# Kernel optimization log

Hardware: AMD Instinct MI355X
Metric: run time of the kernel (lower is better)

Reference implementation:

```python
import jax, jax.numpy as jnp
import numpy as np

B, A, D = 32, 1024, 128
THR = 0.05  # proximity_threshold


def setup_inputs() -> dict:
    key = jax.random.key(0)
    k1, k2, k3, k4, k5 = jax.random.split(key, 5)
    s = 1.0 / np.sqrt(D)
    return {
        "agent_embeds": jax.random.normal(k1, (B, A, D), jnp.float32),
        "agent_coords": jax.random.uniform(k2, (B, A, 2), jnp.float32),
        "agent_mask": jax.random.randint(k3, (B, A), 0, 2).astype(jnp.int32),
        "W1": (jax.random.normal(k4, (D, D), jnp.float32) * s),
        "b1": jnp.zeros((D,), jnp.float32),
        "W2": (jax.random.normal(k5, (D, D), jnp.float32) * s),
        "b2": jnp.zeros((D,), jnp.float32),
    }


def _cluster(coords, valid):
    """Greedy sequential proximity clustering (same order/semantics as the torch loop).
    coords [A,2], valid [A] bool -> assigned [A] int32 (group id; invalid agents = -2)."""
    diff = coords[:, None, :] - coords[None, :, :]          # [A,A,2]
    near_all = jnp.sum(diff * diff, axis=-1) < (THR * THR)   # dist < thr  <=>  dist^2 < thr^2
    assigned0 = jnp.where(valid, -1, -2).astype(jnp.int32)

    def step(carry, i):
        assigned, gid = carry
        start = assigned[i] == -1                 # valid and not yet assigned -> new group
        take = start & near_all[i] & (assigned == -1)  # includes i (dist ii = 0)
        assigned = jnp.where(take, gid, assigned)
        gid = gid + start.astype(jnp.int32)
        return (assigned, gid), None

    (assigned, _), _ = jax.lax.scan(step, (assigned0, jnp.int32(0)), jnp.arange(A))
    return assigned


def reference(agent_embeds, agent_coords, agent_mask, W1, b1, W2, b2):
    valid = agent_mask.astype(bool)                          # [B,A]
    assigned = jax.vmap(_cluster)(agent_coords, valid)       # [B,A] int32

    w = valid.astype(agent_embeds.dtype)                     # [B,A]
    seg = jnp.where(valid, assigned, 0)                      # invalid -> seg 0 with weight 0

    def pool(emb, sg, wt):  # per batch: segment-mean into at most A groups (padded)
        sums = jax.ops.segment_sum(emb * wt[:, None], sg, num_segments=A)  # [A,D]
        cnt = jax.ops.segment_sum(wt, sg, num_segments=A)                  # [A]
        return sums / jnp.maximum(cnt, 1.0)[:, None], cnt > 0

    group_tokens, group_mask = jax.vmap(pool)(agent_embeds, seg, w)  # [B,A,D], [B,A]

    # group_proj MLP applied to the whole (zero-padded) token tensor, as in torch
    h = jax.nn.gelu(group_tokens @ W1 + b1, approximate=False)
    group_tokens = h @ W2 + b2

    agent_to_group = jnp.where(valid, assigned, -1)
    return group_tokens, group_mask, agent_to_group
```

## Files before the change

### kernel.cpp

```cpp
#include <hip/hip_runtime.h>
#include <hip/hip_bf16.h>

#define NB 32
#define NA 1024
#define ND 128
#define TG 16

__device__ __forceinline__ float gelu_exact(float x) {
    return 0.5f * x * (1.0f + erff(x * 0.7071067811865476f));
}

__global__ __launch_bounds__(64, 1) void cluster_kernel(
    const float2* __restrict__ coords, const int* __restrict__ mask,
    int* __restrict__ assigned, int* __restrict__ gcount,
    float* __restrict__ out_mask, float* __restrict__ out_a2g,
    const float* __restrict__ b1, const float* __restrict__ W2,
    const float* __restrict__ b2, float* __restrict__ empty_row)
{
    const int lane = threadIdx.x;

    if (blockIdx.x == NB) {
        __shared__ float h0s[ND];
        h0s[lane]      = gelu_exact(b1[lane]);
        h0s[lane + 64] = gelu_exact(b1[lane + 64]);
        __syncthreads();
        float a0 = b2[lane], a1 = b2[lane + 64];
        for (int k = 0; k < ND; ++k) {
            float h = h0s[k];
            a0 += h * W2[k * ND + lane];
            a1 += h * W2[k * ND + lane + 64];
        }
        empty_row[lane]      = a0;
        empty_row[lane + 64] = a1;
        return;
    }

    const int b = blockIdx.x;
    const float2* cb = coords + (b << 10);
    const int*    mb = mask + (b << 10);

    float2 cxy[16];
    int asg[16];
    unsigned m = 0;
#pragma unroll
    for (int s = 0; s < 16; ++s) {
        cxy[s] = cb[s * 64 + lane];
        int v = mb[s * 64 + lane];
        asg[s] = v ? -1 : -2;
        m |= (v ? 1u : 0u) << s;
    }

    const float thr2 = 0.05f * 0.05f;
    int gid = 0;
#pragma unroll
    for (int s = 0; s < 16; ++s) {
        unsigned long long cand = __ballot((m >> s) & 1u);
        while (cand) {
            int L = (int)__builtin_ctzll(cand);
            float lx = __builtin_bit_cast(float,
                __builtin_amdgcn_readlane(__builtin_bit_cast(int, cxy[s].x), L));
            float ly = __builtin_bit_cast(float,
                __builtin_amdgcn_readlane(__builtin_bit_cast(int, cxy[s].y), L));
            unsigned take = 0u;
#pragma unroll
            for (int t = s; t < 16; ++t) {
                float dx = cxy[t].x - lx;
                float dy = cxy[t].y - ly;
                float d2 = __fadd_rn(__fmul_rn(dx, dx), __fmul_rn(dy, dy));
                bool tk = (d2 < thr2) && ((m >> t) & 1u);
                if (tk) asg[t] = gid;
                take |= (tk ? 1u : 0u) << t;
            }
            m &= ~take;
            ++gid;
            cand = __ballot((m >> s) & 1u);
        }
    }

    int*   ab = assigned + (b << 10);
    float* o2 = out_a2g + (b << 10);
    float* o1 = out_mask + (b << 10);
#pragma unroll
    for (int s = 0; s < 16; ++s) {
        int i = s * 64 + lane;
        ab[i] = asg[s];
        o2[i] = (asg[s] == -2) ? -1.0f : (float)asg[s];
        o1[i] = (i < gid) ? 1.0f : 0.0f;
    }
    if (lane == 0) gcount[b] = gid;
}

__global__ __launch_bounds__(256) void csr_kernel(
    const int* __restrict__ assigned,
    int* __restrict__ memb, int* __restrict__ goff, float* __restrict__ gcntf)
{
    const int b = blockIdx.x;
    const int tid = threadIdx.x;
    __shared__ int cnt[NA];
    __shared__ int sA[NA];
    __shared__ int sB[NA];
    __shared__ int cur[NA];

    for (int i = tid; i < NA; i += 256) cnt[i] = 0;
    __syncthreads();

    const int4 av = ((const int4*)(assigned + (b << 10)))[tid];
    if (av.x >= 0) atomicAdd(&cnt[av.x], 1);
    if (av.y >= 0) atomicAdd(&cnt[av.y], 1);
    if (av.z >= 0) atomicAdd(&cnt[av.z], 1);
    if (av.w >= 0) atomicAdd(&cnt[av.w], 1);
    __syncthreads();

    for (int i = tid; i < NA; i += 256) sA[i] = cnt[i];
    __syncthreads();
    int* src = sA; int* dst = sB;
    for (int d = 1; d < NA; d <<= 1) {
        for (int i = tid; i < NA; i += 256) {
            int v = src[i];
            if (i >= d) v += src[i - d];
            dst[i] = v;
        }
        __syncthreads();
        int* t = src; src = dst; dst = t;
    }
    for (int i = tid; i < NA; i += 256) cur[i] = src[i] - cnt[i];
    __syncthreads();
    for (int i = tid; i < NA; i += 256) {
        goff[(b << 10) + i]  = cur[i];
        gcntf[(b << 10) + i] = (float)cnt[i];
    }
    __syncthreads();

    const int a = tid * 4;
    if (av.x >= 0) { int p = atomicAdd(&cur[av.x], 1); memb[(b << 10) + p] = a; }
    if (av.y >= 0) { int p = atomicAdd(&cur[av.y], 1); memb[(b << 10) + p] = a + 1; }
    if (av.z >= 0) { int p = atomicAdd(&cur[av.z], 1); memb[(b << 10) + p] = a + 2; }
    if (av.w >= 0) { int p = atomicAdd(&cur[av.w], 1); memb[(b << 10) + p] = a + 3; }
}

__global__ __launch_bounds__(256) void token_kernel(
    const float* __restrict__ emb, const int* __restrict__ memb,
    const int* __restrict__ goff, const float* __restrict__ gcntf,
    const int* __restrict__ gcount, float* __restrict__ tokens)
{
    const int b = blockIdx.y;
    if (blockIdx.x * TG >= gcount[b]) return;
    const int g = blockIdx.x * TG + (threadIdx.x >> 4);
    const int sub = threadIdx.x & 15;

    const int off = goff[(b << 10) + g];
    const int n   = (int)gcntf[(b << 10) + g];
    const int* mb = memb + (b << 10) + off;
    const float* eb = emb + ((size_t)(b << 10)) * ND + sub * 8;

    float acc[8];
#pragma unroll
    for (int j = 0; j < 8; ++j) acc[j] = 0.0f;
    for (int k = 0; k < n; ++k) {
        int a = mb[k];
        const float4* e4 = (const float4*)(eb + (size_t)a * ND);
        float4 v0 = e4[0], v1 = e4[1];
        acc[0] += v0.x; acc[1] += v0.y; acc[2] += v0.z; acc[3] += v0.w;
        acc[4] += v1.x; acc[5] += v1.y; acc[6] += v1.z; acc[7] += v1.w;
    }
    const float den = fmaxf((float)n, 1.0f);
    float4 t0, t1;
    t0.x = acc[0] / den; t0.y = acc[1] / den; t0.z = acc[2] / den; t0.w = acc[3] / den;
    t1.x = acc[4] / den; t1.y = acc[5] / den; t1.z = acc[6] / den; t1.w = acc[7] / den;
    float4* tout = (float4*)(tokens + (((size_t)(b << 10)) + g) * ND + sub * 8);
    tout[0] = t0; tout[1] = t1;
}

__global__ __launch_bounds__(256, 2) void mlp_kernel(
    const float* __restrict__ tokens, const int* __restrict__ gcount,
    const float* __restrict__ empty_row,
    const float4* __restrict__ W1, const float* __restrict__ b1,
    const float4* __restrict__ W2, const float* __restrict__ b2,
    float* __restrict__ out0)
{
    const int b = blockIdx.y;
    const int g0 = blockIdx.x * TG;
    const int tid = threadIdx.x;
    float* ob = out0 + ((size_t)(b << 10) + g0) * ND;

    if (g0 >= gcount[b]) {
        float4 r = ((const float4*)empty_row)[tid & 31];
        float4* ob4 = (float4*)ob;
        ob4[tid] = r;
        ob4[tid + 256] = r;
        return;
    }

    __shared__ float4 Wl[4096];
    __shared__ float tok[TG][ND];

    {
        const float4* tsrc = (const float4*)(tokens + ((size_t)(b << 10) + g0) * ND);
        float4* tdst = (float4*)&tok[0][0];
        tdst[tid] = tsrc[tid];
        tdst[tid + 256] = tsrc[tid + 256];
    }
#pragma unroll
    for (int i = 0; i < 16; ++i) Wl[tid + i * 256] = W1[tid + i * 256];
    __syncthreads();

    const int jq = tid & 31;
    const int gs = tid >> 5;
    float acc[2][4];
#pragma unroll
    for (int jj = 0; jj < 4; ++jj) { acc[0][jj] = 0.0f; acc[1][jj] = 0.0f; }

#pragma unroll 4
    for (int dd = 0; dd < ND; ++dd) {
        float4 w = Wl[dd * 32 + jq];
        float t0 = tok[gs][dd];
        float t1 = tok[gs + 8][dd];
        acc[0][0] += t0 * w.x; acc[0][1] += t0 * w.y;
        acc[0][2] += t0 * w.z; acc[0][3] += t0 * w.w;
        acc[1][0] += t1 * w.x; acc[1][1] += t1 * w.y;
        acc[1][2] += t1 * w.z; acc[1][3] += t1 * w.w;
    }
    float4 bb = ((const float4*)b1)[jq];
    __syncthreads();
    {
        float4 h;
        h.x = gelu_exact(acc[0][0] + bb.x);
        h.y = gelu_exact(acc[0][1] + bb.y);
        h.z = gelu_exact(acc[0][2] + bb.z);
        h.w = gelu_exact(acc[0][3] + bb.w);
        *(float4*)&tok[gs][jq * 4] = h;
        h.x = gelu_exact(acc[1][0] + bb.x);
        h.y = gelu_exact(acc[1][1] + bb.y);
        h.z = gelu_exact(acc[1][2] + bb.z);
        h.w = gelu_exact(acc[1][3] + bb.w);
        *(float4*)&tok[gs + 8][jq * 4] = h;
    }
#pragma unroll
    for (int i = 0; i < 16; ++i) Wl[tid + i * 256] = W2[tid + i * 256];
    __syncthreads();

#pragma unroll
    for (int jj = 0; jj < 4; ++jj) { acc[0][jj] = 0.0f; acc[1][jj] = 0.0f; }
#pragma unroll 4
    for (int dd = 0; dd < ND; ++dd) {
        float4 w = Wl[dd * 32 + jq];
        float t0 = tok[gs][dd];
        float t1 = tok[gs + 8][dd];
        acc[0][0] += t0 * w.x; acc[0][1] += t0 * w.y;
        acc[0][2] += t0 * w.z; acc[0][3] += t0 * w.w;
        acc[1][0] += t1 * w.x; acc[1][1] += t1 * w.y;
        acc[1][2] += t1 * w.z; acc[1][3] += t1 * w.w;
    }
    float4 cbv = ((const float4*)b2)[jq];
    {
        float4 o;
        o.x = acc[0][0] + cbv.x; o.y = acc[0][1] + cbv.y;
        o.z = acc[0][2] + cbv.z; o.w = acc[0][3] + cbv.w;
        *(float4*)&ob[(size_t)gs * ND + jq * 4] = o;
        o.x = acc[1][0] + cbv.x; o.y = acc[1][1] + cbv.y;
        o.z = acc[1][2] + cbv.z; o.w = acc[1][3] + cbv.w;
        *(float4*)&ob[(size_t)(gs + 8) * ND + jq * 4] = o;
    }
}

extern "C" void kernel_launch(void* const* d_in, const int* in_sizes, int n_in,
                              void* d_out, int out_size, void* d_ws, size_t ws_size,
                              hipStream_t stream) {
    const float* emb    = (const float*)d_in[0];
    const float* coords = (const float*)d_in[1];
    const int*   mask   = (const int*)d_in[2];
    const float* W1     = (const float*)d_in[3];
    const float* b1     = (const float*)d_in[4];
    const float* W2     = (const float*)d_in[5];
    const float* b2     = (const float*)d_in[6];

    float* out0 = (float*)d_out;
    float* out1 = out0 + (size_t)NB * NA * ND;
    float* out2 = out1 + (size_t)NB * NA;

    float* ws_tok   = (float*)d_ws;
    int*   ws_asg   = (int*)(ws_tok + (size_t)NB * NA * ND);
    int*   ws_memb  = ws_asg + (size_t)NB * NA;
    int*   ws_goff  = ws_memb + (size_t)NB * NA;
    float* ws_gcntf = (float*)(ws_goff + (size_t)NB * NA);
    int*   ws_gcnt  = (int*)(ws_gcntf + (size_t)NB * NA);
    float* ws_empty = (float*)(ws_gcnt + NB);

    cluster_kernel<<<NB + 1, 64, 0, stream>>>(
        (const float2*)coords, mask, ws_asg, ws_gcnt, out1, out2,
        b1, W2, b2, ws_empty);
    csr_kernel<<<NB, 256, 0, stream>>>(ws_asg, ws_memb, ws_goff, ws_gcntf);
    token_kernel<<<dim3(NA / TG, NB), 256, 0, stream>>>(
        emb, ws_memb, ws_goff, ws_gcntf, ws_gcnt, ws_tok);
    mlp_kernel<<<dim3(NA / TG, NB), 256, 0, stream>>>(
        ws_tok, ws_gcnt, ws_empty,
        (const float4*)W1, b1, (const float4*)W2, b2, out0);
}
```

Before: 177.5 us.

## Fuse clustering, CSR build and token pooling into one 1024-thread block

Merges the cluster, CSR and token-pooling kernels into one kernel per batch using 16 waves. Each wave spins on a shared-memory ring of group leaders published by earlier waves, so later waves can filter their agents against existing leaders while earlier waves are still running the sequential greedy pass. The CSR scan and segment-mean pooling then run in the same block from shared memory. This removes two launches and the global round trips for assignments, offsets and members. In exchange, pooling runs on only 32 blocks, and correctness relies on the cross-wave spin-wait ordering.

```diff
diff --git a/kernel.cpp b/kernel.cpp
--- a/kernel.cpp
+++ b/kernel.cpp
@@ -10,165 +10,168 @@
     return 0.5f * x * (1.0f + erff(x * 0.7071067811865476f));
 }
 
-__global__ __launch_bounds__(64, 1) void cluster_kernel(
+__global__ __launch_bounds__(1024, 1) void fused_kernel(
     const float2* __restrict__ coords, const int* __restrict__ mask,
-    int* __restrict__ assigned, int* __restrict__ gcount,
+    const float* __restrict__ emb,
+    int* __restrict__ gcount, float* __restrict__ tokens,
     float* __restrict__ out_mask, float* __restrict__ out_a2g,
     const float* __restrict__ b1, const float* __restrict__ W2,
     const float* __restrict__ b2, float* __restrict__ empty_row)
 {
-    const int lane = threadIdx.x;
+    __shared__ float2 ring[NA + 4];
+    __shared__ int cnt_s[NA];
+    __shared__ int bufA[NA];
+    __shared__ int bufB[NA];
+    __shared__ int memb[NA];
+    __shared__ int done_s[16];
+    __shared__ int lead_cnt;
+
+    const int tid = threadIdx.x;
 
     if (blockIdx.x == NB) {
-        __shared__ float h0s[ND];
-        h0s[lane]      = gelu_exact(b1[lane]);
-        h0s[lane + 64] = gelu_exact(b1[lane + 64]);
+        float* hbuf = (float*)ring;
+        if (tid < ND) hbuf[tid] = gelu_exact(b1[tid]);
         __syncthreads();
-        float a0 = b2[lane], a1 = b2[lane + 64];
-        for (int k = 0; k < ND; ++k) {
-            float h = h0s[k];
-            a0 += h * W2[k * ND + lane];
-            a1 += h * W2[k * ND + lane + 64];
-        }
-        empty_row[lane]      = a0;
-        empty_row[lane + 64] = a1;
+        if (tid < ND) {
+            float acc = b2[tid];
+            for (int k = 0; k < ND; ++k) acc += hbuf[k] * W2[k * ND + tid];
+            empty_row[tid] = acc;
+        }
         return;
     }
 
     const int b = blockIdx.x;
-    const float2* cb = coords + (b << 10);
-    const int*    mb = mask + (b << 10);
-
-    float2 cxy[16];
-    int asg[16];
-    unsigned m = 0;
-#pragma unroll
-    for (int s = 0; s < 16; ++s) {
-        cxy[s] = cb[s * 64 + lane];
-        int v = mb[s * 64 + lane];
-        asg[s] = v ? -1 : -2;
-        m |= (v ? 1u : 0u) << s;
-    }
-
+    const int w = tid >> 6;
+    const int lane = tid & 63;
+
+    if (tid < 16) done_s[tid] = -1;
+    if (tid == 0) lead_cnt = 0;
+
+    float2 p = coords[(b << 10) + tid];
+    const bool valid = mask[(b << 10) + tid] != 0;
+    int asg = valid ? -1 : -2;
+    bool alive = valid;
     const float thr2 = 0.05f * 0.05f;
-    int gid = 0;
-#pragma unroll
-    for (int s = 0; s < 16; ++s) {
-        unsigned long long cand = __ballot((m >> s) & 1u);
-        while (cand) {
-            int L = (int)__builtin_ctzll(cand);
-            float lx = __builtin_bit_cast(float,
-                __builtin_amdgcn_readlane(__builtin_bit_cast(int, cxy[s].x), L));
-            float ly = __builtin_bit_cast(float,
-                __builtin_amdgcn_readlane(__builtin_bit_cast(int, cxy[s].y), L));
-            unsigned take = 0u;
-#pragma unroll
-            for (int t = s; t < 16; ++t) {
-                float dx = cxy[t].x - lx;
-                float dy = cxy[t].y - ly;
-                float d2 = __fadd_rn(__fmul_rn(dx, dx), __fmul_rn(dy, dy));
-                bool tk = (d2 < thr2) && ((m >> t) & 1u);
-                if (tk) asg[t] = gid;
-                take |= (tk ? 1u : 0u) << t;
-            }
-            m &= ~take;
-            ++gid;
-            cand = __ballot((m >> s) & 1u);
-        }
-    }
-
-    int*   ab = assigned + (b << 10);
-    float* o2 = out_a2g + (b << 10);
-    float* o1 = out_mask + (b << 10);
-#pragma unroll
-    for (int s = 0; s < 16; ++s) {
-        int i = s * 64 + lane;
-        ab[i] = asg[s];
-        o2[i] = (asg[s] == -2) ? -1.0f : (float)asg[s];
-        o1[i] = (i < gid) ? 1.0f : 0.0f;
-    }
-    if (lane == 0) gcount[b] = gid;
-}
-
-__global__ __launch_bounds__(256) void csr_kernel(
-    const int* __restrict__ assigned,
-    int* __restrict__ memb, int* __restrict__ goff, float* __restrict__ gcntf)
-{
-    const int b = blockIdx.x;
-    const int tid = threadIdx.x;
-    __shared__ int cnt[NA];
-    __shared__ int sA[NA];
-    __shared__ int sB[NA];
-    __shared__ int cur[NA];
-
-    for (int i = tid; i < NA; i += 256) cnt[i] = 0;
-    __syncthreads();
-
-    const int4 av = ((const int4*)(assigned + (b << 10)))[tid];
-    if (av.x >= 0) atomicAdd(&cnt[av.x], 1);
-    if (av.y >= 0) atomicAdd(&cnt[av.y], 1);
-    if (av.z >= 0) atomicAdd(&cnt[av.z], 1);
-    if (av.w >= 0) atomicAdd(&cnt[av.w], 1);
-    __syncthreads();
-
-    for (int i = tid; i < NA; i += 256) sA[i] = cnt[i];
-    __syncthreads();
-    int* src = sA; int* dst = sB;
+
+    __syncthreads();
+
+    int seen = 0;
+    int target = (w == 0) ? 0 : -1;
+
+    while (true) {
+        int c = __hip_atomic_load(&lead_cnt, __ATOMIC_ACQUIRE,
+                                  __HIP_MEMORY_SCOPE_WORKGROUP);
+        while (seen < c) {
+            float2 l0 = ring[seen];
+            float2 l1 = ring[seen + 1];
+            float2 l2 = ring[seen + 2];
+            float2 l3 = ring[seen + 3];
+            {
+                float dx = p.x - l0.x, dy = p.y - l0.y;
+                float d2 = __fadd_rn(__fmul_rn(dx, dx), __fmul_rn(dy, dy));
+                if (alive && d2 < thr2) { asg = seen; alive = false; }
+            }
+            if (seen + 1 < c) {
+                float dx = p.x - l1.x, dy = p.y - l1.y;
+                float d2 = __fadd_rn(__fmul_rn(dx, dx), __fmul_rn(dy, dy));
+                if (alive && d2 < thr2) { asg = seen + 1; alive = false; }
+            }
+            if (seen + 2 < c) {
+                float dx = p.x - l2.x, dy = p.y - l2.y;
+                float d2 = __fadd_rn(__fmul_rn(dx, dx), __fmul_rn(dy, dy));
+                if (alive && d2 < thr2) { asg = seen + 2; alive = false; }
+            }
+            if (seen + 3 < c) {
+                float dx = p.x - l3.x, dy = p.y - l3.y;
+                float d2 = __fadd_rn(__fmul_rn(dx, dx), __fmul_rn(dy, dy));
+                if (alive && d2 < thr2) { asg = seen + 3; alive = false; }
+            }
+            seen = (seen + 4 < c) ? seen + 4 : c;
+        }
+        if (target < 0)
+            target = __hip_atomic_load(&done_s[w - 1], __ATOMIC_ACQUIRE,
+                                       __HIP_MEMORY_SCOPE_WORKGROUP);
+        if (target >= 0 && seen >= target) break;
+        __builtin_amdgcn_s_sleep(1);
+    }
+
+    __builtin_amdgcn_s_setprio(1);
+    unsigned long long bal;
+    while ((bal = __ballot(alive)) != 0ULL) {
+        const int L = (int)__builtin_ctzll(bal);
+        const float lx = __builtin_bit_cast(float,
+            __builtin_amdgcn_readlane(__builtin_bit_cast(int, p.x), L));
+        const float ly = __builtin_bit_cast(float,
+            __builtin_amdgcn_readlane(__builtin_bit_cast(int, p.y), L));
+        float dx = p.x - lx, dy = p.y - ly;
+        float d2 = __fadd_rn(__fmul_rn(dx, dx), __fmul_rn(dy, dy));
+        bool take = alive && (d2 < thr2);
+        if (take) { asg = seen; alive = false; }
+        if (lane == 0) {
+            ring[seen] = make_float2(lx, ly);
+            __hip_atomic_store(&lead_cnt, seen + 1, __ATOMIC_RELEASE,
+                               __HIP_MEMORY_SCOPE_WORKGROUP);
+        }
+        ++seen;
+    }
+    __builtin_amdgcn_s_setprio(0);
+    if (lane == 0)
+        __hip_atomic_store(&done_s[w], seen, __ATOMIC_RELEASE,
+                           __HIP_MEMORY_SCOPE_WORKGROUP);
+
+    __syncthreads();
+    const int G = lead_cnt;
+
+    cnt_s[tid] = 0;
+    __syncthreads();
+    if (asg >= 0) atomicAdd(&cnt_s[asg], 1);
+    __syncthreads();
+
+    bufA[tid] = cnt_s[tid];
+    __syncthreads();
+    int* src = bufA;
+    int* dst = bufB;
     for (int d = 1; d < NA; d <<= 1) {
-        for (int i = tid; i < NA; i += 256) {
-            int v = src[i];
-            if (i >= d) v += src[i - d];
-            dst[i] = v;
-        }
+        int v = src[tid];
+        if (tid >= d) v += src[tid - d];
+        dst[tid] = v;
         __syncthreads();
-        int* t = src; src = dst; dst = t;
-    }
-    for (int i = tid; i < NA; i += 256) cur[i] = src[i] - cnt[i];
-    __syncthreads();
-    for (int i = tid; i < NA; i += 256) {
-        goff[(b << 10) + i]  = cur[i];
-        gcntf[(b << 10) + i] = (float)cnt[i];
-    }
-    __syncthreads();
-
-    const int a = tid * 4;
-    if (av.x >= 0) { int p = atomicAdd(&cur[av.x], 1); memb[(b << 10) + p] = a; }
-    if (av.y >= 0) { int p = atomicAdd(&cur[av.y], 1); memb[(b << 10) + p] = a + 1; }
-    if (av.z >= 0) { int p = atomicAdd(&cur[av.z], 1); memb[(b << 10) + p] = a + 2; }
-    if (av.w >= 0) { int p = atomicAdd(&cur[av.w], 1); memb[(b << 10) + p] = a + 3; }
-}
-
-__global__ __launch_bounds__(256) void token_kernel(
-    const float* __restrict__ emb, const int* __restrict__ memb,
-    const int* __restrict__ goff, const float* __restrict__ gcntf,
-    const int* __restrict__ gcount, float* __restrict__ tokens)
-{
-    const int b = blockIdx.y;
-    if (blockIdx.x * TG >= gcount[b]) return;
-    const int g = blockIdx.x * TG + (threadIdx.x >> 4);
-    const int sub = threadIdx.x & 15;
-
-    const int off = goff[(b << 10) + g];
-    const int n   = (int)gcntf[(b << 10) + g];
-    const int* mb = memb + (b << 10) + off;
-    const float* eb = emb + ((size_t)(b << 10)) * ND + sub * 8;
-
-    float acc[8];
-#pragma unroll
-    for (int j = 0; j < 8; ++j) acc[j] = 0.0f;
-    for (int k = 0; k < n; ++k) {
-        int a = mb[k];
-        const float4* e4 = (const float4*)(eb + (size_t)a * ND);
-        float4 v0 = e4[0], v1 = e4[1];
-        acc[0] += v0.x; acc[1] += v0.y; acc[2] += v0.z; acc[3] += v0.w;
-        acc[4] += v1.x; acc[5] += v1.y; acc[6] += v1.z; acc[7] += v1.w;
-    }
-    const float den = fmaxf((float)n, 1.0f);
-    float4 t0, t1;
-    t0.x = acc[0] / den; t0.y = acc[1] / den; t0.z = acc[2] / den; t0.w = acc[3] / den;
-    t1.x = acc[4] / den; t1.y = acc[5] / den; t1.z = acc[6] / den; t1.w = acc[7] / den;
-    float4* tout = (float4*)(tokens + (((size_t)(b << 10)) + g) * ND + sub * 8);
-    tout[0] = t0; tout[1] = t1;
+        int* tswap = src; src = dst; dst = tswap;
+    }
+    const int excl = src[tid] - cnt_s[tid];
+    bufB[tid] = excl;
+    bufA[tid] = excl;
+    __syncthreads();
+    if (asg >= 0) {
+        int ppos = atomicAdd(&bufA[asg], 1);
+        memb[ppos] = tid;
+    }
+    __syncthreads();
+
+    out_a2g[(b << 10) + tid] = (asg == -2) ? -1.0f : (float)asg;
+    out_mask[(b << 10) + tid] = (tid < G) ? 1.0f : 0.0f;
+    if (tid == 0) gcount[b] = G;
+
+    const int Gpad = (G + TG - 1) & ~(TG - 1);
+    const float* eb = emb + ((size_t)(b) << 10) * ND;
+    float* tb = tokens + ((size_t)(b) << 10) * ND;
+    for (int g = w; g < Gpad; g += 16) {
+        float a0 = 0.0f, a1 = 0.0f;
+        if (g < G) {
+            const int n = cnt_s[g];
+            const int off = bufB[g];
+            for (int k = 0; k < n; ++k) {
+                const int a = memb[off + k];
+                const float* ea = eb + (size_t)a * ND;
+                a0 += ea[lane];
+                a1 += ea[lane + 64];
+            }
+            const float den = fmaxf((float)n, 1.0f);
+            a0 /= den; a1 /= den;
+        }
+        tb[(size_t)g * ND + lane] = a0;
+        tb[(size_t)g * ND + lane + 64] = a1;
+    }
 }
 
 __global__ __launch_bounds__(256, 2) void mlp_kernel(
@@ -212,13 +215,13 @@
 
 #pragma unroll 4
     for (int dd = 0; dd < ND; ++dd) {
-        float4 w = Wl[dd * 32 + jq];
+        float4 wv = Wl[dd * 32 + jq];
         float t0 = tok[gs][dd];
         float t1 = tok[gs + 8][dd];
-        acc[0][0] += t0 * w.x; acc[0][1] += t0 * w.y;
-        acc[0][2] += t0 * w.z; acc[0][3] += t0 * w.w;
-        acc[1][0] += t1 * w.x; acc[1][1] += t1 * w.y;
-        acc[1][2] += t1 * w.z; acc[1][3] += t1 * w.w;
+        acc[0][0] += t0 * wv.x; acc[0][1] += t0 * wv.y;
+        acc[0][2] += t0 * wv.z; acc[0][3] += t0 * wv.w;
+        acc[1][0] += t1 * wv.x; acc[1][1] += t1 * wv.y;
+        acc[1][2] += t1 * wv.z; acc[1][3] += t1 * wv.w;
     }
     float4 bb = ((const float4*)b1)[jq];
     __syncthreads();
@@ -243,13 +246,13 @@
     for (int jj = 0; jj < 4; ++jj) { acc[0][jj] = 0.0f; acc[1][jj] = 0.0f; }
 #pragma unroll 4
     for (int dd = 0; dd < ND; ++dd) {
-        float4 w = Wl[dd * 32 + jq];
+        float4 wv = Wl[dd * 32 + jq];
         float t0 = tok[gs][dd];
         float t1 = tok[gs + 8][dd];
-        acc[0][0] += t0 * w.x; acc[0][1] += t0 * w.y;
-        acc[0][2] += t0 * w.z; acc[0][3] += t0 * w.w;
-        acc[1][0] += t1 * w.x; acc[1][1] += t1 * w.y;
-        acc[1][2] += t1 * w.z; acc[1][3] += t1 * w.w;
+        acc[0][0] += t0 * wv.x; acc[0][1] += t0 * wv.y;
+        acc[0][2] += t0 * wv.z; acc[0][3] += t0 * wv.w;
+        acc[1][0] += t1 * wv.x; acc[1][1] += t1 * wv.y;
+        acc[1][2] += t1 * wv.z; acc[1][3] += t1 * wv.w;
     }
     float4 cbv = ((const float4*)b2)[jq];
     {
@@ -279,19 +282,13 @@
     float* out2 = out1 + (size_t)NB * NA;
 
     float* ws_tok   = (float*)d_ws;
-    int*   ws_asg   = (int*)(ws_tok + (size_t)NB * NA * ND);
-    int*   ws_memb  = ws_asg + (size_t)NB * NA;
-    int*   ws_goff  = ws_memb + (size_t)NB * NA;
-    float* ws_gcntf = (float*)(ws_goff + (size_t)NB * NA);
-    int*   ws_gcnt  = (int*)(ws_gcntf + (size_t)NB * NA);
+    int*   ws_gcnt  = (int*)(ws_tok + (size_t)NB * NA * ND);
     float* ws_empty = (float*)(ws_gcnt + NB);
 
-    cluster_kernel<<<NB + 1, 64, 0, stream>>>(
-        (const float2*)coords, mask, ws_asg, ws_gcnt, out1, out2,
+    fused_kernel<<<NB + 1, 1024, 0, stream>>>(
+        (const float2*)coords, mask, emb,
+        ws_gcnt, ws_tok, out1, out2,
         b1, W2, b2, ws_empty);
-    csr_kernel<<<NB, 256, 0, stream>>>(ws_asg, ws_memb, ws_goff, ws_gcntf);
-    token_kernel<<<dim3(NA / TG, NB), 256, 0, stream>>>(
-        emb, ws_memb, ws_goff, ws_gcntf, ws_gcnt, ws_tok);
     mlp_kernel<<<dim3(NA / TG, NB), 256, 0, stream>>>(
         ws_tok, ws_gcnt, ws_empty,
         (const float4*)W1, b1, (const float4*)W2, b2, out0);
```

Measured after the change: 147.7 us. 16.8% less time.
